# Kernel tuning notes

Measured on AMD Instinct MI355X. Metric: run time of the kernel, lower is better.

Reference implementation:

```python
import jax, jax.numpy as jnp
import numpy as np

HIDDEN = 256  # C
STE = 128     # D

def setup_inputs() -> dict:
    key = jax.random.key(0)
    ks = jax.random.split(key, 11)
    B, P, Q, N = 8, 96, 96, 1024
    s = 0.02
    return {
        "enc": jax.random.normal(ks[0], (B, P, N, HIDDEN), jnp.float32),
        "ste_enc": jax.random.normal(ks[1], (B, P, N, STE), jnp.float32),
        "ste_dec": jax.random.normal(ks[2], (B, Q, N, STE), jnp.float32),
        "Wq": jax.random.normal(ks[3], (STE, HIDDEN), jnp.float32) * s,
        "bq": jnp.zeros((HIDDEN,), jnp.float32),
        "Wk": jax.random.normal(ks[4], (STE, HIDDEN), jnp.float32) * s,
        "bk": jnp.zeros((HIDDEN,), jnp.float32),
        "Wv": jax.random.normal(ks[5], (HIDDEN, HIDDEN), jnp.float32) * s,
        "bv": jnp.zeros((HIDDEN,), jnp.float32),
        "Wo": jax.random.normal(ks[6], (HIDDEN, HIDDEN), jnp.float32) * s,
        "bo": jnp.zeros((HIDDEN,), jnp.float32),
    }

def reference(enc, ste_enc, ste_dec, Wq, bq, Wk, bk, Wv, bv, Wo, bo):
    # enc: (B,P,N,C), ste_enc: (B,P,N,D), ste_dec: (B,Q,N,D)
    C = enc.shape[-1]
    q = ste_dec @ Wq + bq          # (B,Q,N,H)
    k = ste_enc @ Wk + bk          # (B,P,N,H)
    v = enc @ Wv + bv              # (B,P,N,H)
    # attention per (batch, node): scores (B,N,Q,P)
    scores = jnp.einsum("bqnh,bpnh->bnqp", q, k) / jnp.sqrt(jnp.float32(C))
    attn = jax.nn.softmax(scores, axis=-1)
    out = jnp.einsum("bnqp,bpnh->bqnh", attn, v)  # (B,Q,N,H)
    out = out @ Wo + bo
    return out  # (B,Q,N,C)
```

## Files before the change

### kernel.cpp

```cpp
#include <hip/hip_runtime.h>
#include <stdint.h>

typedef unsigned short u16;
typedef unsigned int u32;
typedef __attribute__((ext_vector_type(8))) short short8;
typedef __attribute__((ext_vector_type(4))) float f32x4;

#define NTHR 384
#define K2E16 0.09016844005556021f

#define KW_OFF    32768
#define KW_STRIDE 272
#define BIAS_OFF  58880
#define BVO_OFF   59264
#define LDS_TOTAL 60288

static __device__ __forceinline__ u16 f2bf(float f) {
  union { float f; u32 u; } v; v.f = f;
  u32 r = v.u + 0x7FFFu + ((v.u >> 16) & 1u);
  return (u16)(r >> 16);
}

__global__ __launch_bounds__(256) void k_setup(
    const float* __restrict__ Wq, const float* __restrict__ Wk,
    const float* __restrict__ Wv, const float* __restrict__ Wo,
    const float* __restrict__ bq,
    const float* __restrict__ bv, const float* __restrict__ bo,
    u16* __restrict__ WkqF, u16* __restrict__ WvoF, float* __restrict__ bvo) {
  const int ci = blockIdx.x;
  const int co = threadIdx.x;
  float acc = 0.f;
  for (int h = 0; h < 256; ++h) acc += Wv[ci*256 + h] * Wo[h*256 + co];
  const int lanepart = ((ci >> 3) & 3)*16 + (co & 15), e = ci & 7;
  const int idxv = (((ci >> 5)*16 + (co >> 4))*64 + lanepart)*8 + e;
  WvoF[idxv] = f2bf(acc);
  if (ci < 128 && co < 144) {
    float a = 0.f;
    if (co < 128)       { for (int h = 0; h < 256; ++h) a += Wk[ci*256 + h] * Wq[co*256 + h]; }
    else if (co == 128) { for (int h = 0; h < 256; ++h) a += Wk[ci*256 + h] * bq[h]; }
    const int idx = (((ci >> 5)*9 + (co >> 4))*64 + lanepart)*8 + e;
    WkqF[idx] = f2bf(a);
  }
  if (ci == 0) {
    float a2 = 0.f;
    for (int h = 0; h < 256; ++h) a2 += bv[h] * Wo[h*256 + co];
    bvo[co] = a2 + bo[co];
  }
}

__global__ __launch_bounds__(NTHR, 3) void k_attn(
    const float* __restrict__ sdec, const float* __restrict__ senc,
    const float* __restrict__ enc,
    const u16* __restrict__ WkqF, const u16* __restrict__ WvoF,
    const float* __restrict__ bvo, float* __restrict__ out) {
  extern __shared__ char smem[];
  char* wvoL   = smem;
  char* kwL    = smem + KW_OFF;
  char* fragA  = smem + KW_OFF;
  char* fragB  = smem;
  float* biasL = (float*)(smem + BIAS_OFF);
  float* bvoL  = (float*)(smem + BVO_OFF);

  const int n = blockIdx.x, b = blockIdx.y;
  const int tid = threadIdx.x, wave = tid >> 6, lane = tid & 63;
  const int g = lane >> 4, c15 = lane & 15;
  const int prow = 16*wave + c15;

  const float* sdp = sdec + ((size_t)((b*96 + prow)*1024 + n))*128 + 8*g;
  const float* sep = senc + ((size_t)((b*96 + prow)*1024 + n))*128 + 8*g;
  float4 sdv[4][2], sev[4][2];
  #pragma unroll
  for (int kt = 0; kt < 4; ++kt) {
    sev[kt][0] = *(const float4*)(sep + 32*kt);
    sev[kt][1] = *(const float4*)(sep + 32*kt + 4);
    sdv[kt][0] = *(const float4*)(sdp + 32*kt);
    sdv[kt][1] = *(const float4*)(sdp + 32*kt + 4);
  }
  const f32x4* wv = (const f32x4*)WvoF;
  f32x4 c0[3];
  #pragma unroll
  for (int i = 0; i < 3; ++i) {
    const int idx = tid + 384*i;
    if (idx < 1024) c0[i] = wv[idx];
  }
  if (tid < 256) bvoL[tid] = bvo[tid];

  short8 sef[4], sdf[4];
  #pragma unroll
  for (int kt = 0; kt < 4; ++kt) {
    union { u32 u[4]; short8 v; } cv;
    cv.u[0] = (u32)f2bf(sev[kt][0].x) | ((u32)f2bf(sev[kt][0].y) << 16);
    cv.u[1] = (u32)f2bf(sev[kt][0].z) | ((u32)f2bf(sev[kt][0].w) << 16);
    cv.u[2] = (u32)f2bf(sev[kt][1].x) | ((u32)f2bf(sev[kt][1].y) << 16);
    cv.u[3] = (u32)f2bf(sev[kt][1].z) | ((u32)f2bf(sev[kt][1].w) << 16);
    sef[kt] = cv.v;
  }
  #pragma unroll
  for (int kt = 0; kt < 4; ++kt) {
    union { u32 u[4]; short8 v; } cv;
    cv.u[0] = (u32)f2bf(sdv[kt][0].x) | ((u32)f2bf(sdv[kt][0].y) << 16);
    cv.u[1] = (u32)f2bf(sdv[kt][0].z) | ((u32)f2bf(sdv[kt][0].w) << 16);
    cv.u[2] = (u32)f2bf(sdv[kt][1].x) | ((u32)f2bf(sdv[kt][1].y) << 16);
    cv.u[3] = (u32)f2bf(sdv[kt][1].z) | ((u32)f2bf(sdv[kt][1].w) << 16);
    sdf[kt] = cv.v;
  }

  {
    f32x4 acc[9];
    #pragma unroll
    for (int nt = 0; nt < 9; ++nt) acc[nt] = (f32x4)0.f;
    #pragma unroll
    for (int kt = 0; kt < 4; ++kt) {
      #pragma unroll
      for (int nt = 0; nt < 9; ++nt) {
        const short8 bf = *(const short8*)(WkqF + (size_t)((kt*9 + nt)*64 + lane)*8);
        acc[nt] = __builtin_amdgcn_mfma_f32_16x16x32_bf16(sef[kt], bf, acc[nt], 0, 0, 0);
      }
    }
    #pragma unroll
    for (int nt = 0; nt < 8; ++nt) {
      #pragma unroll
      for (int r = 0; r < 4; ++r)
        *(u16*)(kwL + (16*wave + 4*g + r)*KW_STRIDE + 2*(c15 + 16*nt)) = f2bf(acc[nt][r]);
    }
    if (c15 == 0) {
      #pragma unroll
      for (int r = 0; r < 4; ++r) biasL[16*wave + 4*g + r] = acc[8][r];
    }
  }
  {
    f32x4* b0 = (f32x4*)wvoL;
    #pragma unroll
    for (int i = 0; i < 3; ++i) {
      const int idx = tid + 384*i;
      if (idx < 1024) b0[idx] = c0[i];
    }
  }
  __syncthreads();

  const float* ep = enc + ((size_t)((b*96 + prow)*1024 + n))*256 + 8*g;
  float4 evr[4][2];
  #pragma unroll
  for (int kt = 0; kt < 4; ++kt) {
    evr[kt][0] = *(const float4*)(ep + 32*kt);
    evr[kt][1] = *(const float4*)(ep + 32*kt + 4);
  }

  f32x4 sac[6];
  #pragma unroll
  for (int pt = 0; pt < 6; ++pt) sac[pt] = (f32x4)0.f;
  #pragma unroll
  for (int kt = 0; kt < 4; ++kt) {
    #pragma unroll
    for (int pt = 0; pt < 6; ++pt) {
      const short8 kf = *(const short8*)(kwL + (16*pt + c15)*KW_STRIDE + 16*g + 64*kt);
      sac[pt] = __builtin_amdgcn_mfma_f32_16x16x32_bf16(kf, sdf[kt], sac[pt], 0, 0, 0);
    }
  }
  #pragma unroll
  for (int pt = 0; pt < 6; ++pt)
    #pragma unroll
    for (int r = 0; r < 4; ++r)
      sac[pt][r] += biasL[16*pt + 4*g + r];

  float m = sac[0][0];
  #pragma unroll
  for (int pt = 0; pt < 6; ++pt)
    #pragma unroll
    for (int r = 0; r < 4; ++r) m = fmaxf(m, sac[pt][r]);
  m = fmaxf(m, __shfl_xor(m, 16));
  m = fmaxf(m, __shfl_xor(m, 32));
  float s = 0.f;
  #pragma unroll
  for (int pt = 0; pt < 6; ++pt)
    #pragma unroll
    for (int r = 0; r < 4; ++r) {
      const float e = exp2f((sac[pt][r] - m) * K2E16);
      sac[pt][r] = e; s += e;
    }
  s += __shfl_xor(s, 16);
  s += __shfl_xor(s, 32);
  const float rs = 1.f / s;

  short8 af[3];
  #pragma unroll
  for (int kb = 0; kb < 3; ++kb) {
    union { u32 u[4]; short8 v; } cv;
    cv.u[0] = (u32)f2bf(sac[2*kb][0]*rs)   | ((u32)f2bf(sac[2*kb][1]*rs)   << 16);
    cv.u[1] = (u32)f2bf(sac[2*kb][2]*rs)   | ((u32)f2bf(sac[2*kb][3]*rs)   << 16);
    cv.u[2] = (u32)f2bf(sac[2*kb+1][0]*rs) | ((u32)f2bf(sac[2*kb+1][1]*rs) << 16);
    cv.u[3] = (u32)f2bf(sac[2*kb+1][2]*rs) | ((u32)f2bf(sac[2*kb+1][3]*rs) << 16);
    af[kb] = cv.v;
  }

  f32x4 acc2[16];
  #pragma unroll
  for (int nt = 0; nt < 16; ++nt) acc2[nt] = (f32x4)0.f;
  #pragma unroll
  for (int kt = 0; kt < 8; ++kt) {
    f32x4 nx[3];
    if (kt < 7) {
      const f32x4* src = wv + (kt + 1)*1024;
      #pragma unroll
      for (int i = 0; i < 3; ++i) {
        const int idx = tid + 384*i;
        if (idx < 1024) nx[i] = src[idx];
      }
    }
    union { u32 u[4]; short8 v; } cv;
    cv.u[0] = (u32)f2bf(evr[kt & 3][0].x) | ((u32)f2bf(evr[kt & 3][0].y) << 16);
    cv.u[1] = (u32)f2bf(evr[kt & 3][0].z) | ((u32)f2bf(evr[kt & 3][0].w) << 16);
    cv.u[2] = (u32)f2bf(evr[kt & 3][1].x) | ((u32)f2bf(evr[kt & 3][1].y) << 16);
    cv.u[3] = (u32)f2bf(evr[kt & 3][1].z) | ((u32)f2bf(evr[kt & 3][1].w) << 16);
    const short8 a = cv.v;
    if (kt < 4) {
      evr[kt & 3][0] = *(const float4*)(ep + 32*(kt + 4));
      evr[kt & 3][1] = *(const float4*)(ep + 32*(kt + 4) + 4);
    }
    const char* buf = wvoL + (kt & 1)*16384;
    #pragma unroll
    for (int nt = 0; nt < 16; ++nt) {
      const short8 bf = *(const short8*)(buf + ((nt*64 + lane) << 4));
      acc2[nt] = __builtin_amdgcn_mfma_f32_16x16x32_bf16(a, bf, acc2[nt], 0, 0, 0);
    }
    if (kt < 7) {
      f32x4* bw = (f32x4*)(wvoL + ((kt + 1) & 1)*16384);
      #pragma unroll
      for (int i = 0; i < 3; ++i) {
        const int idx = tid + 384*i;
        if (idx < 1024) bw[idx] = nx[i];
      }
    }
    __syncthreads();
  }

  const int kb0 = wave >> 1, hi = wave & 1;
  #pragma unroll
  for (int ntl = 0; ntl < 8; ++ntl) {
    uint2 oA, oB;
    const f32x4 vA = acc2[ntl], vB = acc2[8 + ntl];
    oA.x = (u32)f2bf(vA[0]) | ((u32)f2bf(vA[1]) << 16);
    oA.y = (u32)f2bf(vA[2]) | ((u32)f2bf(vA[3]) << 16);
    oB.x = (u32)f2bf(vB[0]) | ((u32)f2bf(vB[1]) << 16);
    oB.y = (u32)f2bf(vB[2]) | ((u32)f2bf(vB[3]) << 16);
    *(uint2*)(fragA + (((ntl*3 + kb0)*64 + lane) << 4) + hi*8) = oA;
    *(uint2*)(fragB + (((ntl*3 + kb0)*64 + lane) << 4) + hi*8) = oB;
  }
  __syncthreads();

  #pragma unroll
  for (int nt = 0; nt < 16; ++nt) {
    const char* fb = (nt < 8) ? fragA : fragB;
    const int ntl = nt & 7;
    f32x4 oa = (f32x4)0.f;
    #pragma unroll
    for (int kb = 0; kb < 3; ++kb) {
      const short8 ef = *(const short8*)(fb + (((ntl*3 + kb)*64 + lane) << 4));
      oa = __builtin_amdgcn_mfma_f32_16x16x32_bf16(af[kb], ef, oa, 0, 0, 0);
    }
    const int c = c15 + 16*nt;
    const float bz = bvoL[c];
    #pragma unroll
    for (int r = 0; r < 4; ++r) {
      const int qi = 16*wave + 4*g + r;
      out[((size_t)((b*96 + qi)*1024 + n))*256 + c] = oa[r] + bz;
    }
  }
}

extern "C" void kernel_launch(void* const* d_in, const int* in_sizes, int n_in,
                              void* d_out, int out_size, void* d_ws, size_t ws_size,
                              hipStream_t stream) {
  const float* enc     = (const float*)d_in[0];
  const float* ste_enc = (const float*)d_in[1];
  const float* ste_dec = (const float*)d_in[2];
  const float* Wq = (const float*)d_in[3];
  const float* bq = (const float*)d_in[4];
  const float* Wk = (const float*)d_in[5];
  const float* Wv = (const float*)d_in[7];
  const float* bv = (const float*)d_in[8];
  const float* Wo = (const float*)d_in[9];
  const float* bo = (const float*)d_in[10];
  float* out = (float*)d_out;

  u16*   WkqF = (u16*)d_ws;
  u16*   WvoF = (u16*)((char*)d_ws + 36864);
  float* bvo  = (float*)((char*)d_ws + 167936);

  k_setup<<<dim3(256), dim3(256), 0, stream>>>(Wq, Wk, Wv, Wo, bq, bv, bo,
                                               WkqF, WvoF, bvo);
  k_attn<<<dim3(1024, 8), dim3(NTHR), LDS_TOTAL, stream>>>(
      ste_dec, ste_enc, enc, WkqF, WvoF, bvo, out);
}
```

Measured before the change: 643.6 us.

## Stage Wkq in LDS and deepen Wvo global prefetch to two tiles

Stages the first 8 column tiles of the fused Wk·Wq weight in shared memory before the key-weight MFMA loop, so each wave stops re-reading them from global memory; only the bias tile still comes from global. The Wvo weight prefetch becomes two register stages deep, alternating pf0 and pf1 buffers, so global loads are issued two k-steps ahead of their LDS store. This needs extra registers, so the occupancy hint drops from 3 to 2 blocks per SM, and it adds two extra __syncthreads.

```diff
diff --git a/kernel.cpp b/kernel.cpp
--- a/kernel.cpp
+++ b/kernel.cpp
@@ -48,7 +48,7 @@
   }
 }
 
-__global__ __launch_bounds__(NTHR, 3) void k_attn(
+__global__ __launch_bounds__(NTHR, 2) void k_attn(
     const float* __restrict__ sdec, const float* __restrict__ senc,
     const float* __restrict__ enc,
     const u16* __restrict__ WkqF, const u16* __restrict__ WvoF,
@@ -66,6 +66,15 @@
   const int g = lane >> 4, c15 = lane & 15;
   const int prow = 16*wave + c15;
 
+  f32x4 wkq[6];
+  #pragma unroll
+  for (int i = 0; i < 6; ++i) {
+    const int idx = tid + 384*i;
+    if (idx < 2048) {
+      const int f = idx >> 6, l = idx & 63;
+      wkq[i] = ((const f32x4*)WkqF)[((f >> 3)*9 + (f & 7))*64 + l];
+    }
+  }
   const float* sdp = sdec + ((size_t)((b*96 + prow)*1024 + n))*128 + 8*g;
   const float* sep = senc + ((size_t)((b*96 + prow)*1024 + n))*128 + 8*g;
   float4 sdv[4][2], sev[4][2];
@@ -84,6 +93,16 @@
     if (idx < 1024) c0[i] = wv[idx];
   }
   if (tid < 256) bvoL[tid] = bvo[tid];
+
+  {
+    f32x4* d = (f32x4*)wvoL;
+    #pragma unroll
+    for (int i = 0; i < 6; ++i) {
+      const int idx = tid + 384*i;
+      if (idx < 2048) d[idx] = wkq[i];
+    }
+  }
+  __syncthreads();
 
   short8 sef[4], sdf[4];
   #pragma unroll
@@ -112,10 +131,12 @@
     #pragma unroll
     for (int kt = 0; kt < 4; ++kt) {
       #pragma unroll
-      for (int nt = 0; nt < 9; ++nt) {
-        const short8 bf = *(const short8*)(WkqF + (size_t)((kt*9 + nt)*64 + lane)*8);
+      for (int nt = 0; nt < 8; ++nt) {
+        const short8 bf = *(const short8*)(wvoL + ((kt*8 + nt)*64 + lane)*16);
         acc[nt] = __builtin_amdgcn_mfma_f32_16x16x32_bf16(sef[kt], bf, acc[nt], 0, 0, 0);
       }
+      const short8 bf8 = *(const short8*)(WkqF + (size_t)((kt*9 + 8)*64 + lane)*8);
+      acc[8] = __builtin_amdgcn_mfma_f32_16x16x32_bf16(sef[kt], bf8, acc[8], 0, 0, 0);
     }
     #pragma unroll
     for (int nt = 0; nt < 8; ++nt) {
@@ -128,6 +149,8 @@
       for (int r = 0; r < 4; ++r) biasL[16*wave + 4*g + r] = acc[8][r];
     }
   }
+  __syncthreads();
+
   {
     f32x4* b0 = (f32x4*)wvoL;
     #pragma unroll
@@ -136,8 +159,12 @@
       if (idx < 1024) b0[idx] = c0[i];
     }
   }
-  __syncthreads();
-
+  f32x4 pf0[3], pf1[3];
+  #pragma unroll
+  for (int i = 0; i < 3; ++i) {
+    const int idx = tid + 384*i;
+    if (idx < 1024) pf0[i] = wv[1024 + idx];
+  }
   const float* ep = enc + ((size_t)((b*96 + prow)*1024 + n))*256 + 8*g;
   float4 evr[4][2];
   #pragma unroll
@@ -192,19 +219,21 @@
     cv.u[3] = (u32)f2bf(sac[2*kb+1][2]*rs) | ((u32)f2bf(sac[2*kb+1][3]*rs) << 16);
     af[kb] = cv.v;
   }
+  __syncthreads();
 
   f32x4 acc2[16];
   #pragma unroll
   for (int nt = 0; nt < 16; ++nt) acc2[nt] = (f32x4)0.f;
   #pragma unroll
   for (int kt = 0; kt < 8; ++kt) {
-    f32x4 nx[3];
-    if (kt < 7) {
-      const f32x4* src = wv + (kt + 1)*1024;
-      #pragma unroll
-      for (int i = 0; i < 3; ++i) {
-        const int idx = tid + 384*i;
-        if (idx < 1024) nx[i] = src[idx];
+    if (kt < 6) {
+      const f32x4* src = wv + (kt + 2)*1024;
+      if (((kt + 1) & 1) == 0) {
+        #pragma unroll
+        for (int i = 0; i < 3; ++i) { const int idx = tid + 384*i; if (idx < 1024) pf0[i] = src[idx]; }
+      } else {
+        #pragma unroll
+        for (int i = 0; i < 3; ++i) { const int idx = tid + 384*i; if (idx < 1024) pf1[i] = src[idx]; }
       }
     }
     union { u32 u[4]; short8 v; } cv;
@@ -225,10 +254,12 @@
     }
     if (kt < 7) {
       f32x4* bw = (f32x4*)(wvoL + ((kt + 1) & 1)*16384);
-      #pragma unroll
-      for (int i = 0; i < 3; ++i) {
-        const int idx = tid + 384*i;
-        if (idx < 1024) bw[idx] = nx[i];
+      if ((kt & 1) == 0) {
+        #pragma unroll
+        for (int i = 0; i < 3; ++i) { const int idx = tid + 384*i; if (idx < 1024) bw[idx] = pf0[i]; }
+      } else {
+        #pragma unroll
+        for (int i = 0; i < 3; ++i) { const int idx = tid + 384*i; if (idx < 1024) bw[idx] = pf1[i]; }
       }
     }
     __syncthreads();
```

After: 608.9 us. -5.4%, faster.
